# Optimization experiments

Hardware: AMD Instinct MI355X
Metric: run time of the kernel (lower is better)

Reference implementation:

```python
import jax, jax.numpy as jnp
from jax import lax
import numpy as np


def setup_inputs() -> dict:
    key = jax.random.key(0)
    k1, k2, k3, k4, k5 = jax.random.split(key, 5)
    bs, m, v, L, P = 2, 16, 16, 40320, 32
    preds = jax.random.normal(k1, (bs, m, v, L), dtype=jnp.float32)
    target = jax.random.normal(k2, (bs, v, L), dtype=jnp.float32)
    weights = jax.random.uniform(k3, (L,), dtype=jnp.float32)
    scale = jax.random.uniform(k4, (v,), dtype=jnp.float32)
    # binary-ish patch masks over grid points (float, as in the torch buffer)
    masks = (jax.random.uniform(k5, (P, L)) < 0.25).astype(jnp.float32)
    return {"preds": preds, "target": target, "weights": weights,
            "scale": scale, "masks": masks, "beta": 1}


def _energy_score(x, y, m, beta):
    # x: (bs, m, D) ensemble, y: (bs, D) observation
    diff = x - y[:, None, :]
    a = jnp.sqrt(jnp.sum(diff * diff, axis=-1))            # (bs, m)
    score_a = jnp.mean(jnp.sum(a ** beta, axis=-1)) / m
    # pairwise distances via Gram trick (cdist p=2)
    sq = jnp.sum(x * x, axis=-1)                            # (bs, m)
    g = jnp.einsum('bid,bjd->bij', x, x)                    # (bs, m, m)
    d2 = jnp.maximum(sq[:, :, None] + sq[:, None, :] - 2.0 * g, 0.0)
    pos = d2 > 0
    d = jnp.where(pos, jnp.sqrt(jnp.where(pos, d2, 1.0)), 0.0)
    score_b = jnp.mean(jnp.sum(d ** beta, axis=(1, 2))) / (2 * m * (m - 1))
    return score_a - score_b


def reference(preds, target, weights, scale, masks, beta):
    beta = float(beta)
    bs, m, v, L = preds.shape
    # buffer scaling as in forward()
    p = preds * scale[None, None, :, None] * weights        # (bs, m, v, L)
    t = target * scale[None, :, None] * weights             # (bs, v, L)

    def body(acc, mask):
        # rearrange 'bs m v latlon -> bs m (latlon v)'
        x = (p * mask).transpose(0, 1, 3, 2).reshape(bs, m, L * v)
        y = (t * mask).transpose(0, 2, 1).reshape(bs, L * v)
        return acc + _energy_score(x, y, m, beta), None

    total, _ = lax.scan(body, jnp.float32(0.0), masks)
    return total
```

## Files before the change

kernel.cpp:

```cpp
#include <hip/hip_runtime.h>
#include <math.h>

#define BS 2
#define M 16
#define V 16
#define NROWB 136
#define NROWS 272
#define PMASK 32
#define NPB 315
#define CH 2
#define NE 8704
#define PBSTRIDE 8704

typedef __attribute__((ext_vector_type(8))) short bf16x8;
typedef __attribute__((ext_vector_type(4))) float f32x4;
typedef __attribute__((ext_vector_type(4))) unsigned int u32x4;

static __device__ __forceinline__ unsigned short f2bf(float x) {
    unsigned int u = __float_as_uint(x);
    unsigned int r = (u + 0x7FFFu + ((u >> 16) & 1u)) >> 16;
    return (unsigned short)r;
}

static __device__ __forceinline__ void k1_stage(
    const float* __restrict__ preds, float* __restrict__ dst,
    int b, int v0, int l0, int L, int lane, int wave)
{
#pragma unroll
    for (int n = 0; n < 4; ++n) {
        int r0 = wave * 16 + n * 4;
        int r = r0 + (lane >> 4);
        int grow = b * 256 + (r >> 2) * 16 + v0 + (r & 3);
        const float* g = preds + (size_t)grow * L + l0 + (lane & 15) * 4;
        __builtin_amdgcn_global_load_lds(
            (const __attribute__((address_space(1))) unsigned int*)g,
            (__attribute__((address_space(3))) unsigned int*)(dst + r0 * 64),
            16, 0, 0);
    }
}

template<int W>
static __device__ __forceinline__ void k1_chunk(
    const float* __restrict__ xsb,
    const float* __restrict__ targ,
    const float* __restrict__ scl,
    float wl,
    int v0, int lane, float* __restrict__ acc)
{
    const int base = (W == 0) ? 0 : 34 * W - 16;
    const int npair = (W == 0) ? 18 : 34;
    const int aoff = (W == 0) ? 16 : 0;

#pragma unroll
    for (int vc = 0; vc < 4; ++vc) {
        const int v = v0 + vc;
        float s = scl[v] * wl;
        float x[M];
#pragma unroll
        for (int i = 0; i < M; ++i)
            x[i] = xsb[(i * 4 + vc) * 64 + lane] * s;
        if (W == 0) {
            float y = targ[v] * s;
#pragma unroll
            for (int i = 0; i < M; ++i) {
                float d = x[i] - y;
                acc[i] = fmaf(d, d, acc[i]);
            }
        }
        int k = 0;
#pragma unroll
        for (int i = 0; i < M; ++i) {
#pragma unroll
            for (int j = i + 1; j < M; ++j) {
                if (k >= base && k < base + npair) {
                    float d = x[i] - x[j];
                    acc[aoff + k - base] = fmaf(d, d, acc[aoff + k - base]);
                }
                ++k;
            }
        }
    }
}

__global__ __launch_bounds__(256, 2)
void k1_fused(const float* __restrict__ preds, const float* __restrict__ target,
              const float* __restrict__ weights, const float* __restrict__ scale,
              const float* __restrict__ masks, float* __restrict__ partial,
              float* __restrict__ out, int L)
{
    __shared__ float xs[2][4096];
    __shared__ unsigned short sld[144 * 64];

    const int t = (int)threadIdx.x;
    const int lane = t & 63, wave = t >> 6;
    const int pb = (int)blockIdx.x;
    const int b  = (int)blockIdx.y;

    if (pb == 0 && b == 0 && t == 0) out[0] = 0.0f;

    ((unsigned int*)sld)[136 * 32 + t] = 0;

    k1_stage(preds, &xs[0][0], b, 0, pb * 64, L, lane, wave);

    float scl[V];
#pragma unroll
    for (int v = 0; v < V; ++v) scl[v] = scale[v];
    float wl = weights[pb * 64 + lane];
    float targ[V];
    if (wave == 0) {
#pragma unroll
        for (int v = 0; v < V; ++v)
            targ[v] = target[(size_t)(b * V + v) * L + pb * 64 + lane];
    }

    const int ntile = (wave == 3) ? 3 : 2;
    f32x4 pacc[3][2];
#pragma unroll
    for (int ti = 0; ti < 3; ++ti)
#pragma unroll
        for (int pt = 0; pt < 2; ++pt)
            pacc[ti][pt] = (f32x4){0.f, 0.f, 0.f, 0.f};

    float acc[34];
#pragma unroll
    for (int r = 0; r < 34; ++r) acc[r] = 0.0f;

#pragma unroll
    for (int c = 0; c < CH; ++c) {
        const int l0 = (pb + NPB * c) * 64;
#pragma unroll
        for (int vq = 0; vq < 4; ++vq) {
            const int s = c * 4 + vq;
            __syncthreads();
            if (s + 1 < 4 * CH) {
                const int ns = s + 1;
                k1_stage(preds, &xs[ns & 1][0], b, (ns & 3) * 4,
                         (pb + NPB * (ns >> 2)) * 64, L, lane, wave);
            }
            if (c > 0 && vq == 0) {
                wl = weights[l0 + lane];
                if (wave == 0) {
#pragma unroll
                    for (int v = 0; v < V; ++v)
                        targ[v] = target[(size_t)(b * V + v) * L + l0 + lane];
                }
#pragma unroll
                for (int r = 0; r < 34; ++r) acc[r] = 0.0f;
            }
            const float* xsb = &xs[s & 1][0];
            switch (wave) {
                case 0: k1_chunk<0>(xsb, targ, scl, wl, vq * 4, lane, acc); break;
                case 1: k1_chunk<1>(xsb, targ, scl, wl, vq * 4, lane, acc); break;
                case 2: k1_chunk<2>(xsb, targ, scl, wl, vq * 4, lane, acc); break;
                default: k1_chunk<3>(xsb, targ, scl, wl, vq * 4, lane, acc); break;
            }
        }

#pragma unroll
        for (int r = 0; r < 34; ++r) {
            const int R = 34 * wave + r;
            sld[R * 64 + (lane ^ ((R & 7) << 3))] = f2bf(acc[r]);
        }
        __syncthreads();

#pragma unroll
        for (int ks = 0; ks < 2; ++ks) {
            bf16x8 bfr[2];
#pragma unroll
            for (int pt = 0; pt < 2; ++pt) {
                const float* mp = masks + (size_t)(pt * 16 + (lane & 15)) * L
                                + l0 + ks * 32 + (lane >> 4) * 8;
                u32x4 m0 = *(const u32x4*)mp;
                u32x4 m1 = *(const u32x4*)(mp + 4);
                union { unsigned int u[4]; bf16x8 v; } bb;
                bb.u[0] = __builtin_amdgcn_perm(m0.y, m0.x, 0x07060302);
                bb.u[1] = __builtin_amdgcn_perm(m0.w, m0.z, 0x07060302);
                bb.u[2] = __builtin_amdgcn_perm(m1.y, m1.x, 0x07060302);
                bb.u[3] = __builtin_amdgcn_perm(m1.w, m1.z, 0x07060302);
                bfr[pt] = bb.v;
            }
#pragma unroll
            for (int ti = 0; ti < 3; ++ti) {
                if (ti >= ntile) continue;
                const int tile = (ti == 2) ? 8 : (wave + ti * 4);
                const bf16x8 a = *(const bf16x8*)&sld[
                    (tile * 16 + (lane & 15)) * 64 +
                    ((ks * 32 + (lane >> 4) * 8) ^ ((lane & 7) << 3))];
                pacc[ti][0] = __builtin_amdgcn_mfma_f32_16x16x32_bf16(
                    a, bfr[0], pacc[ti][0], 0, 0, 0);
                pacc[ti][1] = __builtin_amdgcn_mfma_f32_16x16x32_bf16(
                    a, bfr[1], pacc[ti][1], 0, 0, 0);
            }
        }
    }

    float* P = partial + (size_t)(pb * 2 + b) * (NROWB * PMASK);
#pragma unroll
    for (int ti = 0; ti < 3; ++ti) {
        if (ti >= ntile) continue;
        const int tile = (ti == 2) ? 8 : (wave + ti * 4);
#pragma unroll
        for (int pt = 0; pt < 2; ++pt)
#pragma unroll
            for (int reg = 0; reg < 4; ++reg) {
                const int row = tile * 16 + (lane >> 4) * 4 + reg;
                if (row < NROWB)
                    P[row * 32 + pt * 16 + (lane & 15)] = pacc[ti][pt][reg];
            }
    }
}

__global__ __launch_bounds__(256, 2)
void k3_finalize(const float* __restrict__ P, const int* __restrict__ beta_p,
                 float* __restrict__ out)
{
    const int t = (int)threadIdx.x;
    const int e = (int)blockIdx.x * 256 + t;

    float a0 = 0.f, a1 = 0.f, a2 = 0.f, a3 = 0.f, a4 = 0.f;
    const float* p = P + e;
    for (int q = 0; q < NPB; q += 5) {
        a0 += p[(size_t)(q    ) * PBSTRIDE];
        a1 += p[(size_t)(q + 1) * PBSTRIDE];
        a2 += p[(size_t)(q + 2) * PBSTRIDE];
        a3 += p[(size_t)(q + 3) * PBSTRIDE];
        a4 += p[(size_t)(q + 4) * PBSTRIDE];
    }
    float d2 = fmaxf(((a0 + a1) + (a2 + a3)) + a4, 0.0f);
    float beta = (float)beta_p[0];
    float d = (beta == 1.0f) ? sqrtf(d2) : powf(d2, 0.5f * beta);

    const float wa = 1.0f / (float)(BS * M);
    const float wb = -1.0f / (float)(BS * M * (M - 1));
    const int row_g = e >> 5;
    const int local = row_g % NROWB;
    float sum = ((local < M) ? wa : wb) * d;

    const int lane = t & 63, wv = t >> 6;
#pragma unroll
    for (int off = 32; off > 0; off >>= 1)
        sum += __shfl_down(sum, off, 64);
    __shared__ float red[4];
    if (lane == 0) red[wv] = sum;
    __syncthreads();
    if (t == 0)
        atomicAdd(out, red[0] + red[1] + red[2] + red[3]);
}

extern "C" void kernel_launch(void* const* d_in, const int* in_sizes, int n_in,
                              void* d_out, int out_size, void* d_ws, size_t ws_size,
                              hipStream_t stream)
{
    const float* preds   = (const float*)d_in[0];
    const float* target  = (const float*)d_in[1];
    const float* weights = (const float*)d_in[2];
    const float* scale   = (const float*)d_in[3];
    const float* masks   = (const float*)d_in[4];
    const int*   beta    = (const int*)d_in[5];
    float* out = (float*)d_out;

    int L = in_sizes[2];

    float* partial = (float*)d_ws;

    dim3 g1(NPB, BS);
    k1_fused<<<g1, 256, 0, stream>>>(preds, target, weights, scale, masks,
                                     partial, out, L);

    k3_finalize<<<NE / 256, 256, 0, stream>>>(partial, beta, out);
}
```

Before: 178.1 us.

## Double k1 grid to one tile per block and split final reduction into two stages

The main kernel now launches twice as many blocks, each handling a single 64-point chunk with half-width (2-variable) staging steps instead of two chunks with 4-variable steps. This shrinks shared memory per block and gives more blocks to spread across CUs. Because the partial buffer doubles, the single-pass finalize is replaced by a split reduction (30 slices of 21 blocks each) followed by a small finalize kernel, adding a launch and an intermediate buffer round trip.

```diff
diff --git a/kernel.cpp b/kernel.cpp
--- a/kernel.cpp
+++ b/kernel.cpp
@@ -7,10 +7,11 @@
 #define NROWB 136
 #define NROWS 272
 #define PMASK 32
-#define NPB 315
-#define CH 2
+#define NPB 630
 #define NE 8704
 #define PBSTRIDE 8704
+#define SPLIT 30
+#define QPB 21
 
 typedef __attribute__((ext_vector_type(8))) short bf16x8;
 typedef __attribute__((ext_vector_type(4))) float f32x4;
@@ -27,10 +28,10 @@
     int b, int v0, int l0, int L, int lane, int wave)
 {
 #pragma unroll
-    for (int n = 0; n < 4; ++n) {
-        int r0 = wave * 16 + n * 4;
+    for (int n = 0; n < 2; ++n) {
+        int r0 = wave * 8 + n * 4;
         int r = r0 + (lane >> 4);
-        int grow = b * 256 + (r >> 2) * 16 + v0 + (r & 3);
+        int grow = b * 256 + (r >> 1) * 16 + v0 + (r & 1);
         const float* g = preds + (size_t)grow * L + l0 + (lane & 15) * 4;
         __builtin_amdgcn_global_load_lds(
             (const __attribute__((address_space(1))) unsigned int*)g,
@@ -52,13 +53,13 @@
     const int aoff = (W == 0) ? 16 : 0;
 
 #pragma unroll
-    for (int vc = 0; vc < 4; ++vc) {
+    for (int vc = 0; vc < 2; ++vc) {
         const int v = v0 + vc;
         float s = scl[v] * wl;
         float x[M];
 #pragma unroll
         for (int i = 0; i < M; ++i)
-            x[i] = xsb[(i * 4 + vc) * 64 + lane] * s;
+            x[i] = xsb[(i * 2 + vc) * 64 + lane] * s;
         if (W == 0) {
             float y = targ[v] * s;
 #pragma unroll
@@ -88,30 +89,56 @@
               const float* __restrict__ masks, float* __restrict__ partial,
               float* __restrict__ out, int L)
 {
-    __shared__ float xs[2][4096];
+    __shared__ float xs[2][2048];
     __shared__ unsigned short sld[144 * 64];
 
     const int t = (int)threadIdx.x;
     const int lane = t & 63, wave = t >> 6;
     const int pb = (int)blockIdx.x;
     const int b  = (int)blockIdx.y;
+    const int l0 = pb * 64;
 
     if (pb == 0 && b == 0 && t == 0) out[0] = 0.0f;
 
     ((unsigned int*)sld)[136 * 32 + t] = 0;
 
-    k1_stage(preds, &xs[0][0], b, 0, pb * 64, L, lane, wave);
+    k1_stage(preds, &xs[0][0], b, 0, l0, L, lane, wave);
 
     float scl[V];
 #pragma unroll
     for (int v = 0; v < V; ++v) scl[v] = scale[v];
-    float wl = weights[pb * 64 + lane];
+    float wl = weights[l0 + lane];
     float targ[V];
     if (wave == 0) {
 #pragma unroll
         for (int v = 0; v < V; ++v)
-            targ[v] = target[(size_t)(b * V + v) * L + pb * 64 + lane];
-    }
+            targ[v] = target[(size_t)(b * V + v) * L + l0 + lane];
+    }
+
+    float acc[34];
+#pragma unroll
+    for (int r = 0; r < 34; ++r) acc[r] = 0.0f;
+
+#pragma unroll
+    for (int s = 0; s < 8; ++s) {
+        __syncthreads();
+        if (s < 7)
+            k1_stage(preds, &xs[(s + 1) & 1][0], b, (s + 1) * 2, l0, L, lane, wave);
+        const float* xsb = &xs[s & 1][0];
+        switch (wave) {
+            case 0: k1_chunk<0>(xsb, targ, scl, wl, s * 2, lane, acc); break;
+            case 1: k1_chunk<1>(xsb, targ, scl, wl, s * 2, lane, acc); break;
+            case 2: k1_chunk<2>(xsb, targ, scl, wl, s * 2, lane, acc); break;
+            default: k1_chunk<3>(xsb, targ, scl, wl, s * 2, lane, acc); break;
+        }
+    }
+
+#pragma unroll
+    for (int r = 0; r < 34; ++r) {
+        const int R = 34 * wave + r;
+        sld[R * 64 + (lane ^ ((R & 7) << 3))] = f2bf(acc[r]);
+    }
+    __syncthreads();
 
     const int ntile = (wave == 3) ? 3 : 2;
     f32x4 pacc[3][2];
@@ -121,76 +148,33 @@
         for (int pt = 0; pt < 2; ++pt)
             pacc[ti][pt] = (f32x4){0.f, 0.f, 0.f, 0.f};
 
-    float acc[34];
-#pragma unroll
-    for (int r = 0; r < 34; ++r) acc[r] = 0.0f;
-
-#pragma unroll
-    for (int c = 0; c < CH; ++c) {
-        const int l0 = (pb + NPB * c) * 64;
-#pragma unroll
-        for (int vq = 0; vq < 4; ++vq) {
-            const int s = c * 4 + vq;
-            __syncthreads();
-            if (s + 1 < 4 * CH) {
-                const int ns = s + 1;
-                k1_stage(preds, &xs[ns & 1][0], b, (ns & 3) * 4,
-                         (pb + NPB * (ns >> 2)) * 64, L, lane, wave);
-            }
-            if (c > 0 && vq == 0) {
-                wl = weights[l0 + lane];
-                if (wave == 0) {
-#pragma unroll
-                    for (int v = 0; v < V; ++v)
-                        targ[v] = target[(size_t)(b * V + v) * L + l0 + lane];
-                }
-#pragma unroll
-                for (int r = 0; r < 34; ++r) acc[r] = 0.0f;
-            }
-            const float* xsb = &xs[s & 1][0];
-            switch (wave) {
-                case 0: k1_chunk<0>(xsb, targ, scl, wl, vq * 4, lane, acc); break;
-                case 1: k1_chunk<1>(xsb, targ, scl, wl, vq * 4, lane, acc); break;
-                case 2: k1_chunk<2>(xsb, targ, scl, wl, vq * 4, lane, acc); break;
-                default: k1_chunk<3>(xsb, targ, scl, wl, vq * 4, lane, acc); break;
-            }
-        }
-
-#pragma unroll
-        for (int r = 0; r < 34; ++r) {
-            const int R = 34 * wave + r;
-            sld[R * 64 + (lane ^ ((R & 7) << 3))] = f2bf(acc[r]);
-        }
-        __syncthreads();
-
-#pragma unroll
-        for (int ks = 0; ks < 2; ++ks) {
-            bf16x8 bfr[2];
-#pragma unroll
-            for (int pt = 0; pt < 2; ++pt) {
-                const float* mp = masks + (size_t)(pt * 16 + (lane & 15)) * L
-                                + l0 + ks * 32 + (lane >> 4) * 8;
-                u32x4 m0 = *(const u32x4*)mp;
-                u32x4 m1 = *(const u32x4*)(mp + 4);
-                union { unsigned int u[4]; bf16x8 v; } bb;
-                bb.u[0] = __builtin_amdgcn_perm(m0.y, m0.x, 0x07060302);
-                bb.u[1] = __builtin_amdgcn_perm(m0.w, m0.z, 0x07060302);
-                bb.u[2] = __builtin_amdgcn_perm(m1.y, m1.x, 0x07060302);
-                bb.u[3] = __builtin_amdgcn_perm(m1.w, m1.z, 0x07060302);
-                bfr[pt] = bb.v;
-            }
-#pragma unroll
-            for (int ti = 0; ti < 3; ++ti) {
-                if (ti >= ntile) continue;
-                const int tile = (ti == 2) ? 8 : (wave + ti * 4);
-                const bf16x8 a = *(const bf16x8*)&sld[
-                    (tile * 16 + (lane & 15)) * 64 +
-                    ((ks * 32 + (lane >> 4) * 8) ^ ((lane & 7) << 3))];
-                pacc[ti][0] = __builtin_amdgcn_mfma_f32_16x16x32_bf16(
-                    a, bfr[0], pacc[ti][0], 0, 0, 0);
-                pacc[ti][1] = __builtin_amdgcn_mfma_f32_16x16x32_bf16(
-                    a, bfr[1], pacc[ti][1], 0, 0, 0);
-            }
+#pragma unroll
+    for (int ks = 0; ks < 2; ++ks) {
+        bf16x8 bfr[2];
+#pragma unroll
+        for (int pt = 0; pt < 2; ++pt) {
+            const float* mp = masks + (size_t)(pt * 16 + (lane & 15)) * L
+                            + l0 + ks * 32 + (lane >> 4) * 8;
+            u32x4 m0 = *(const u32x4*)mp;
+            u32x4 m1 = *(const u32x4*)(mp + 4);
+            union { unsigned int u[4]; bf16x8 v; } bb;
+            bb.u[0] = __builtin_amdgcn_perm(m0.y, m0.x, 0x07060302);
+            bb.u[1] = __builtin_amdgcn_perm(m0.w, m0.z, 0x07060302);
+            bb.u[2] = __builtin_amdgcn_perm(m1.y, m1.x, 0x07060302);
+            bb.u[3] = __builtin_amdgcn_perm(m1.w, m1.z, 0x07060302);
+            bfr[pt] = bb.v;
+        }
+#pragma unroll
+        for (int ti = 0; ti < 3; ++ti) {
+            if (ti >= ntile) continue;
+            const int tile = (ti == 2) ? 8 : (wave + ti * 4);
+            const bf16x8 a = *(const bf16x8*)&sld[
+                (tile * 16 + (lane & 15)) * 64 +
+                ((ks * 32 + (lane >> 4) * 8) ^ ((lane & 7) << 3))];
+            pacc[ti][0] = __builtin_amdgcn_mfma_f32_16x16x32_bf16(
+                a, bfr[0], pacc[ti][0], 0, 0, 0);
+            pacc[ti][1] = __builtin_amdgcn_mfma_f32_16x16x32_bf16(
+                a, bfr[1], pacc[ti][1], 0, 0, 0);
         }
     }
 
@@ -211,22 +195,38 @@
 }
 
 __global__ __launch_bounds__(256, 2)
-void k3_finalize(const float* __restrict__ P, const int* __restrict__ beta_p,
-                 float* __restrict__ out)
+void k3a_reduce(const float* __restrict__ P, float* __restrict__ P2)
 {
     const int t = (int)threadIdx.x;
     const int e = (int)blockIdx.x * 256 + t;
-
-    float a0 = 0.f, a1 = 0.f, a2 = 0.f, a3 = 0.f, a4 = 0.f;
-    const float* p = P + e;
-    for (int q = 0; q < NPB; q += 5) {
+    const int spl = (int)blockIdx.y;
+
+    const float* p = P + (size_t)(spl * QPB) * PBSTRIDE + e;
+    float a0 = 0.f, a1 = 0.f, a2 = 0.f;
+#pragma unroll
+    for (int q = 0; q < QPB; q += 3) {
         a0 += p[(size_t)(q    ) * PBSTRIDE];
         a1 += p[(size_t)(q + 1) * PBSTRIDE];
         a2 += p[(size_t)(q + 2) * PBSTRIDE];
-        a3 += p[(size_t)(q + 3) * PBSTRIDE];
-        a4 += p[(size_t)(q + 4) * PBSTRIDE];
-    }
-    float d2 = fmaxf(((a0 + a1) + (a2 + a3)) + a4, 0.0f);
+    }
+    P2[(size_t)spl * NE + e] = (a0 + a1) + a2;
+}
+
+__global__ __launch_bounds__(256, 2)
+void k3b_finalize(const float* __restrict__ P2, const int* __restrict__ beta_p,
+                  float* __restrict__ out)
+{
+    const int t = (int)threadIdx.x;
+    const int e = (int)blockIdx.x * 256 + t;
+
+    float a0 = 0.f, a1 = 0.f, a2 = 0.f;
+#pragma unroll
+    for (int q = 0; q < SPLIT; q += 3) {
+        a0 += P2[(size_t)(q    ) * NE + e];
+        a1 += P2[(size_t)(q + 1) * NE + e];
+        a2 += P2[(size_t)(q + 2) * NE + e];
+    }
+    float d2 = fmaxf((a0 + a1) + a2, 0.0f);
     float beta = (float)beta_p[0];
     float d = (beta == 1.0f) ? sqrtf(d2) : powf(d2, 0.5f * beta);
 
@@ -262,10 +262,15 @@
     int L = in_sizes[2];
 
     float* partial = (float*)d_ws;
+    size_t p_bytes = (size_t)NPB * 2 * NROWB * PMASK * sizeof(float);
+    float* partial2 = (float*)((char*)d_ws + ((p_bytes + 255) & ~(size_t)255));
 
     dim3 g1(NPB, BS);
     k1_fused<<<g1, 256, 0, stream>>>(preds, target, weights, scale, masks,
                                      partial, out, L);
 
-    k3_finalize<<<NE / 256, 256, 0, stream>>>(partial, beta, out);
-}
+    dim3 g3a(NE / 256, SPLIT);
+    k3a_reduce<<<g3a, 256, 0, stream>>>(partial, partial2);
+
+    k3b_finalize<<<NE / 256, 256, 0, stream>>>(partial2, beta, out);
+}
```

After: 152.5 us. -14.4%, faster.
